# Optimization experiments

Measured on AMD Instinct MI355X. Metric: run time of the kernel, lower is better.

The kernel has to match this reference:

```python
import jax, jax.numpy as jnp
import numpy as np

N, D = 8192, 4096

def setup_inputs() -> dict:
    key = jax.random.key(0)
    obs_scores = jax.random.normal(key, (N, D), dtype=jnp.float32)
    return {"obs_scores": obs_scores}

def reference(obs_scores) -> jnp.ndarray:
    # loss = sum_{i<j} ||x_i - x_j||^2
    #      = N * sum_i ||x_i||^2 - || sum_i x_i ||^2   (closed-form rewrite)
    n = obs_scores.shape[0]
    sq_norms_total = jnp.sum(obs_scores * obs_scores)          # sum_i ||x_i||^2
    col_sum = jnp.sum(obs_scores, axis=0)                      # sum_i x_i  (shape [D])
    loss = n * sq_norms_total - jnp.sum(col_sum * col_sum)
    return loss
```

## Files before the change

kernel.cpp:

```cpp
#include <hip/hip_runtime.h>


#define NROWS 8192
#define NCOLS 4096

constexpr int BLOCK = 256;
constexpr int GRID  = 512;
constexpr int F4_PER_ROW = NCOLS / 4;
constexpr int K = F4_PER_ROW / BLOCK;

__global__ __launch_bounds__(BLOCK) void stability_partial(
    const float* __restrict__ x, float* __restrict__ ws)
{
    const int t = threadIdx.x;

    float4 cs[K];
    #pragma unroll
    for (int k = 0; k < K; ++k) cs[k] = make_float4(0.f, 0.f, 0.f, 0.f);
    float ss = 0.f;

    for (int r = blockIdx.x; r < NROWS; r += gridDim.x) {
        const float4* row = reinterpret_cast<const float4*>(x + (size_t)r * NCOLS);
        #pragma unroll
        for (int k = 0; k < K; ++k) {
            float4 v = row[t + k * BLOCK];
            cs[k].x += v.x; cs[k].y += v.y; cs[k].z += v.z; cs[k].w += v.w;
            ss += v.x * v.x + v.y * v.y + v.z * v.z + v.w * v.w;
        }
    }

    #pragma unroll
    for (int k = 0; k < K; ++k) {
        const int c = 4 * (t + k * BLOCK);
        atomicAdd(&ws[c + 0], cs[k].x);
        atomicAdd(&ws[c + 1], cs[k].y);
        atomicAdd(&ws[c + 2], cs[k].z);
        atomicAdd(&ws[c + 3], cs[k].w);
    }

    #pragma unroll
    for (int off = 32; off > 0; off >>= 1) ss += __shfl_down(ss, off, 64);
    __shared__ float wss[BLOCK / 64];
    if ((t & 63) == 0) wss[t >> 6] = ss;
    __syncthreads();
    if (t == 0) {
        float s = 0.f;
        #pragma unroll
        for (int w = 0; w < BLOCK / 64; ++w) s += wss[w];
        atomicAdd(&ws[NCOLS], s);
    }
}

__global__ __launch_bounds__(BLOCK) void stability_finalize(
    const float* __restrict__ ws, float* __restrict__ out)
{
    const int t = threadIdx.x;
    float acc = 0.f;
    #pragma unroll
    for (int k = 0; k < NCOLS / BLOCK; ++k) {
        float c = ws[t + k * BLOCK];
        acc += c * c;
    }
    #pragma unroll
    for (int off = 32; off > 0; off >>= 1) acc += __shfl_down(acc, off, 64);
    __shared__ float wss[BLOCK / 64];
    if ((t & 63) == 0) wss[t >> 6] = acc;
    __syncthreads();
    if (t == 0) {
        float colsq = 0.f;
        #pragma unroll
        for (int w = 0; w < BLOCK / 64; ++w) colsq += wss[w];
        out[0] = (float)NROWS * ws[NCOLS] - colsq;
    }
}

extern "C" void kernel_launch(void* const* d_in, const int* in_sizes, int n_in,
                              void* d_out, int out_size, void* d_ws, size_t ws_size,
                              hipStream_t stream) {
    const float* x = (const float*)d_in[0];
    float* ws  = (float*)d_ws;
    float* out = (float*)d_out;

    hipMemsetAsync(ws, 0, (NCOLS + 1) * sizeof(float), stream);

    stability_partial<<<GRID, BLOCK, 0, stream>>>(x, ws);
    stability_finalize<<<1, BLOCK, 0, stream>>>(ws, out);
}
```

Measured before the change: 244.9 us.

## Replace atomic column reduction with per-block partials and a two-stage reduction

Each block now owns a contiguous slab of 16 rows and writes its column partial sums and square-sum to a workspace array instead of issuing atomics. A second kernel reduces the partials per column and squares them, and a third combines the results. This removes the memset and the global float atomics, and batches four rows of loads per iteration to keep more memory requests in flight. In exchange it writes and re-reads an 8 MB partials buffer and adds an extra launch, and it falls back to the old path if the workspace is too small.

```diff
diff --git a/kernel.cpp b/kernel.cpp
--- a/kernel.cpp
+++ b/kernel.cpp
@@ -5,39 +5,121 @@
 #define NCOLS 4096
 
 constexpr int BLOCK = 256;
-constexpr int GRID  = 512;
-constexpr int F4_PER_ROW = NCOLS / 4;
-constexpr int K = F4_PER_ROW / BLOCK;
+constexpr int PB    = 512;
+constexpr int RPB   = NROWS / PB;
+constexpr int CQB   = 64;
+constexpr size_t P_ELEMS = (size_t)PB * NCOLS;
+constexpr size_t SS_OFF  = P_ELEMS;
+constexpr size_t CQ_OFF  = P_ELEMS + PB;
+constexpr size_t WS_NEEDED = (P_ELEMS + PB + CQB) * sizeof(float);
 
-__global__ __launch_bounds__(BLOCK) void stability_partial(
+__global__ __launch_bounds__(BLOCK) void s1_partials(
+    const float* __restrict__ x, float* __restrict__ ws)
+{
+    const int t = threadIdx.x, b = blockIdx.x;
+    float4 cs[4];
+    #pragma unroll
+    for (int k = 0; k < 4; ++k) cs[k] = make_float4(0.f, 0.f, 0.f, 0.f);
+    float ss = 0.f;
+
+    const float* base = x + (size_t)b * RPB * NCOLS;
+    #pragma unroll
+    for (int rr = 0; rr < RPB; rr += 4) {
+        float4 v[16];
+        #pragma unroll
+        for (int r = 0; r < 4; ++r) {
+            const float4* row = reinterpret_cast<const float4*>(
+                base + (size_t)(rr + r) * NCOLS);
+            #pragma unroll
+            for (int k = 0; k < 4; ++k) v[r * 4 + k] = row[t + k * BLOCK];
+        }
+        #pragma unroll
+        for (int k = 0; k < 16; ++k) {
+            const int c = k & 3;
+            cs[c].x += v[k].x; cs[c].y += v[k].y; cs[c].z += v[k].z; cs[c].w += v[k].w;
+            ss += v[k].x * v[k].x + v[k].y * v[k].y + v[k].z * v[k].z + v[k].w * v[k].w;
+        }
+    }
+
+    float4* P = reinterpret_cast<float4*>(ws) + (size_t)b * (NCOLS / 4);
+    #pragma unroll
+    for (int k = 0; k < 4; ++k) P[t + k * BLOCK] = cs[k];
+
+    #pragma unroll
+    for (int off = 32; off > 0; off >>= 1) ss += __shfl_down(ss, off, 64);
+    __shared__ float wss[BLOCK / 64];
+    if ((t & 63) == 0) wss[t >> 6] = ss;
+    __syncthreads();
+    if (t == 0) ws[SS_OFF + b] = wss[0] + wss[1] + wss[2] + wss[3];
+}
+
+__global__ __launch_bounds__(BLOCK) void s2_colsq(
+    const float* __restrict__ ws, float* __restrict__ wcq)
+{
+    const int t = threadIdx.x;
+    const int tj = t & 63, tp = t >> 6;
+    const int j = blockIdx.x * 64 + tj;
+    float c = 0.f;
+    #pragma unroll 8
+    for (int p = tp; p < PB; p += 4) c += ws[(size_t)p * NCOLS + j];
+    __shared__ float part[4][64];
+    part[tp][tj] = c;
+    __syncthreads();
+    if (t < 64) {
+        float cj = part[0][tj] + part[1][tj] + part[2][tj] + part[3][tj];
+        float v = cj * cj;
+        #pragma unroll
+        for (int off = 32; off > 0; off >>= 1) v += __shfl_down(v, off, 64);
+        if (tj == 0) wcq[blockIdx.x] = v;
+    }
+}
+
+__global__ __launch_bounds__(BLOCK) void s3_final(
+    const float* __restrict__ ws, float* __restrict__ out)
+{
+    const int t = threadIdx.x;
+    float ssp = ws[SS_OFF + t] + ws[SS_OFF + BLOCK + t];
+    float cqp = (t < CQB) ? ws[CQ_OFF + t] : 0.f;
+    #pragma unroll
+    for (int off = 32; off > 0; off >>= 1) {
+        ssp += __shfl_down(ssp, off, 64);
+        cqp += __shfl_down(cqp, off, 64);
+    }
+    __shared__ float wa[BLOCK / 64], wb[BLOCK / 64];
+    if ((t & 63) == 0) { wa[t >> 6] = ssp; wb[t >> 6] = cqp; }
+    __syncthreads();
+    if (t == 0) {
+        float sstot = wa[0] + wa[1] + wa[2] + wa[3];
+        float cqtot = wb[0] + wb[1] + wb[2] + wb[3];
+        out[0] = (float)NROWS * sstot - cqtot;
+    }
+}
+
+__global__ __launch_bounds__(BLOCK) void fb_partial(
     const float* __restrict__ x, float* __restrict__ ws)
 {
     const int t = threadIdx.x;
-
-    float4 cs[K];
+    float4 cs[4];
     #pragma unroll
-    for (int k = 0; k < K; ++k) cs[k] = make_float4(0.f, 0.f, 0.f, 0.f);
+    for (int k = 0; k < 4; ++k) cs[k] = make_float4(0.f, 0.f, 0.f, 0.f);
     float ss = 0.f;
-
     for (int r = blockIdx.x; r < NROWS; r += gridDim.x) {
         const float4* row = reinterpret_cast<const float4*>(x + (size_t)r * NCOLS);
         #pragma unroll
-        for (int k = 0; k < K; ++k) {
+        for (int k = 0; k < 4; ++k) {
             float4 v = row[t + k * BLOCK];
             cs[k].x += v.x; cs[k].y += v.y; cs[k].z += v.z; cs[k].w += v.w;
             ss += v.x * v.x + v.y * v.y + v.z * v.z + v.w * v.w;
         }
     }
-
     #pragma unroll
-    for (int k = 0; k < K; ++k) {
+    for (int k = 0; k < 4; ++k) {
         const int c = 4 * (t + k * BLOCK);
         atomicAdd(&ws[c + 0], cs[k].x);
         atomicAdd(&ws[c + 1], cs[k].y);
         atomicAdd(&ws[c + 2], cs[k].z);
         atomicAdd(&ws[c + 3], cs[k].w);
     }
-
     #pragma unroll
     for (int off = 32; off > 0; off >>= 1) ss += __shfl_down(ss, off, 64);
     __shared__ float wss[BLOCK / 64];
@@ -51,7 +133,7 @@
     }
 }
 
-__global__ __launch_bounds__(BLOCK) void stability_finalize(
+__global__ __launch_bounds__(BLOCK) void fb_finalize(
     const float* __restrict__ ws, float* __restrict__ out)
 {
     const int t = threadIdx.x;
@@ -81,8 +163,13 @@
     float* ws  = (float*)d_ws;
     float* out = (float*)d_out;
 
-    hipMemsetAsync(ws, 0, (NCOLS + 1) * sizeof(float), stream);
-
-    stability_partial<<<GRID, BLOCK, 0, stream>>>(x, ws);
-    stability_finalize<<<1, BLOCK, 0, stream>>>(ws, out);
+    if (ws_size >= WS_NEEDED) {
+        s1_partials<<<PB, BLOCK, 0, stream>>>(x, ws);
+        s2_colsq<<<CQB, BLOCK, 0, stream>>>(ws, ws + CQ_OFF);
+        s3_final<<<1, BLOCK, 0, stream>>>(ws, out);
+    } else {
+        hipMemsetAsync(ws, 0, (NCOLS + 1) * sizeof(float), stream);
+        fb_partial<<<512, BLOCK, 0, stream>>>(x, ws);
+        fb_finalize<<<1, BLOCK, 0, stream>>>(ws, out);
+    }
 }
```

Result: faster. 201.7 us (-17.6%).
